# Kernel optimization log

Measured on AMD Instinct MI355X. Metric: run time of the kernel, lower is better.

## Reference

```python
import jax, jax.numpy as jnp
import numpy as np

NUM_HEADS = 16

def setup_inputs() -> dict:
    key = jax.random.key(0)
    k1, k2, k3, k4 = jax.random.split(key, 4)
    B, N, C = 4, 2048, 1024
    x = jax.random.normal(k1, (B, N, C), dtype=jnp.float32)
    xpos = jax.random.randint(k2, (B, N), 0, 2048, dtype=jnp.int64)
    Wqkv = jax.random.normal(k3, (C, 3 * C), dtype=jnp.float32) * (C ** -0.5)
    Wproj = jax.random.normal(k4, (C, C), dtype=jnp.float32) * (C ** -0.5)
    bproj = jnp.zeros((C,), dtype=jnp.float32)
    return {"x": x, "xpos": xpos, "Wqkv": Wqkv, "Wproj": Wproj, "bproj": bproj}

def reference(x, xpos, Wqkv, Wproj, bproj):
    # rope is None in this configuration, so xpos is unused (matches torch default path).
    B, N, C = x.shape
    H = NUM_HEADS
    Dh = C // H
    scale = Dh ** -0.5
    qkv = jnp.einsum('bnc,cd->bnd', x, Wqkv)              # [B, N, 3C]
    qkv = qkv.reshape(B, N, 3, H, Dh)
    q, k, v = qkv[:, :, 0], qkv[:, :, 1], qkv[:, :, 2]    # [B, N, H, Dh]
    scores = jnp.einsum('bnhd,bmhd->bhnm', q, k) * scale  # [B, H, N, N]
    attn = jax.nn.softmax(scores, axis=-1)
    out = jnp.einsum('bhnm,bmhd->bnhd', attn, v)          # [B, N, H, Dh]
    out = out.reshape(B, N, C)
    return jnp.einsum('bnc,cd->bnd', out, Wproj) + bproj
```

## Files before the change

kernel.cpp:

```cpp
#include <hip/hip_runtime.h>
#include <stdint.h>

#define DEVINL __device__ __forceinline__

typedef __bf16 bf16x8 __attribute__((ext_vector_type(8)));
typedef float f32x4 __attribute__((ext_vector_type(4)));
typedef float f32x16 __attribute__((ext_vector_type(16)));
typedef uint32_t u32x4 __attribute__((ext_vector_type(4)));

DEVINL uint16_t f2bf(float f) {
    uint32_t u = __builtin_bit_cast(uint32_t, f);
    uint32_t r = (u + 0x7FFFu + ((u >> 16) & 1u)) >> 16;
    return (uint16_t)r;
}

DEVINL bf16x8 ld8(const uint16_t* p) {
    u32x4 v = *(const u32x4*)p;
    return __builtin_bit_cast(bf16x8, v);
}

DEVINL void gload16(const void* g, void* l) {
    __builtin_amdgcn_global_load_lds(
        (const __attribute__((address_space(1))) uint32_t*)g,
        (__attribute__((address_space(3))) uint32_t*)l, 16, 0, 0);
}

DEVINL uint32_t cvtpk(float lo, float hi) {
    uint32_t r;
    asm("v_cvt_pk_bf16_f32 %0, %1, %2" : "=v"(r) : "v"(lo), "v"(hi));
    return r;
}

DEVINL float exp2_fast(float x) {
    float r;
    asm("v_exp_f32 %0, %1" : "=v"(r) : "v"(x));
    return r;
}

__global__ void k_cvt_x(const float* __restrict__ x, uint16_t* __restrict__ xb, int n8) {
    int i = blockIdx.x * blockDim.x + threadIdx.x;
    if (i >= n8) return;
    const float4* src = (const float4*)x + (size_t)i * 2;
    float4 a = src[0], b = src[1];
    union { uint16_t u[8]; u32x4 v; } o;
    o.u[0] = f2bf(a.x); o.u[1] = f2bf(a.y); o.u[2] = f2bf(a.z); o.u[3] = f2bf(a.w);
    o.u[4] = f2bf(b.x); o.u[5] = f2bf(b.y); o.u[6] = f2bf(b.z); o.u[7] = f2bf(b.w);
    ((u32x4*)xb)[i] = o.v;
}

__global__ void k_transW(const float* __restrict__ W, uint16_t* __restrict__ WT, int Nn) {
    __shared__ uint16_t t[64 * 65];
    int k0 = blockIdx.y * 64, n0 = blockIdx.x * 64;
    int tid = threadIdx.x;
#pragma unroll
    for (int i = 0; i < 4; ++i) {
        int c = tid + i * 256;
        int kr = c >> 4, nc = c & 15;
        float4 v = *(const float4*)(W + (size_t)(k0 + kr) * Nn + n0 + nc * 4);
        t[(nc * 4 + 0) * 65 + kr] = f2bf(v.x);
        t[(nc * 4 + 1) * 65 + kr] = f2bf(v.y);
        t[(nc * 4 + 2) * 65 + kr] = f2bf(v.z);
        t[(nc * 4 + 3) * 65 + kr] = f2bf(v.w);
    }
    __syncthreads();
#pragma unroll
    for (int i = 0; i < 2; ++i) {
        int c = tid + i * 256;
        int nr = c >> 3, kc = c & 7;
        union { uint16_t u[8]; u32x4 v; } o;
#pragma unroll
        for (int j = 0; j < 8; ++j) o.u[j] = t[nr * 65 + kc * 8 + j];
        *(u32x4*)(WT + (size_t)(n0 + nr) * 1024 + k0 + kc * 8) = o.v;
    }
}

__global__ void k_transV(const uint16_t* __restrict__ vn, uint16_t* __restrict__ vt) {
    __shared__ uint16_t t[64 * 65];
    int bh = blockIdx.y;
    int n0 = blockIdx.x * 64;
    int tid = threadIdx.x;
#pragma unroll
    for (int i = 0; i < 2; ++i) {
        int c = tid + i * 256;
        int n = c >> 3, dc = c & 7;
        u32x4 vv = *(const u32x4*)(vn + ((size_t)bh * 2048 + n0 + n) * 64 + dc * 8);
        union { u32x4 v4; uint16_t u[8]; } in; in.v4 = vv;
#pragma unroll
        for (int j = 0; j < 8; ++j) t[(dc * 8 + j) * 65 + n] = in.u[j];
    }
    __syncthreads();
#pragma unroll
    for (int i = 0; i < 2; ++i) {
        int c = tid + i * 256;
        int dh = c >> 3, nc = c & 7;
        union { uint16_t u[8]; u32x4 v4; } o;
#pragma unroll
        for (int j = 0; j < 8; ++j) o.u[j] = t[dh * 65 + nc * 8 + j];
        *(u32x4*)(vt + ((size_t)bh * 64 + dh) * 2048 + n0 + nc * 8) = o.v4;
    }
}

template <int MODE>
__global__ __launch_bounds__(256) void k_gemm(
    const uint16_t* __restrict__ A, const uint16_t* __restrict__ BT,
    const float* __restrict__ bias,
    uint16_t* __restrict__ qo, uint16_t* __restrict__ ko, uint16_t* __restrict__ vo,
    float* __restrict__ out) {
    __shared__ uint16_t a_lds[128 * 64];
    __shared__ uint16_t b_lds[128 * 64];
    int tid = threadIdx.x;
    int w = tid >> 6, l = tid & 63;
    int l15 = l & 15, l4 = l >> 4;
    int m0 = blockIdx.y * 128, n0 = blockIdx.x * 128;
    int wr = w >> 1, wc = w & 1;
    f32x4 acc[4][4] = {};

    for (int kt = 0; kt < 16; ++kt) {
#pragma unroll
        for (int i = 0; i < 4; ++i) {
            int c = i * 256 + w * 64 + l;
            int row = c >> 3, slot = c & 7;
            int kc = slot ^ (row & 7);
            gload16(A + (size_t)(m0 + row) * 1024 + kt * 64 + kc * 8,
                    a_lds + (size_t)(i * 256 + w * 64) * 8);
            gload16(BT + (size_t)(n0 + row) * 1024 + kt * 64 + kc * 8,
                    b_lds + (size_t)(i * 256 + w * 64) * 8);
        }
        __syncthreads();
#pragma unroll
        for (int kkk = 0; kkk < 2; ++kkk) {
            bf16x8 af[4], bfr[4];
#pragma unroll
            for (int i = 0; i < 4; ++i) {
                int row = wr * 64 + i * 16 + l15;
                af[i] = ld8(a_lds + row * 64 + ((kkk * 4 + l4) ^ (row & 7)) * 8);
                int rowb = wc * 64 + i * 16 + l15;
                bfr[i] = ld8(b_lds + rowb * 64 + ((kkk * 4 + l4) ^ (rowb & 7)) * 8);
            }
#pragma unroll
            for (int i = 0; i < 4; ++i)
#pragma unroll
                for (int j = 0; j < 4; ++j)
                    acc[i][j] = __builtin_amdgcn_mfma_f32_16x16x32_bf16(
                        af[i], bfr[j], acc[i][j], 0, 0, 0);
        }
        __syncthreads();
    }

    if constexpr (MODE == 0) {
#pragma unroll
        for (int i = 0; i < 4; ++i)
#pragma unroll
            for (int j = 0; j < 4; ++j) {
                int d = n0 + wc * 64 + j * 16 + l15;
                int s = d >> 10, h = (d >> 6) & 15, dh = d & 63;
                uint16_t* dst0 = (s == 0) ? qo : (s == 1) ? ko : vo;
                float sc = (s == 0) ? 0.18033688011112042f : 1.0f;
#pragma unroll
                for (int r = 0; r < 4; ++r) {
                    int m = m0 + wr * 64 + i * 16 + l4 * 4 + r;
                    int b = m >> 11, n = m & 2047;
                    dst0[((size_t)(b * 16 + h) * 2048 + n) * 64 + dh] = f2bf(acc[i][j][r] * sc);
                }
            }
    } else {
#pragma unroll
        for (int j = 0; j < 4; ++j) {
            int d = n0 + wc * 64 + j * 16 + l15;
            float bv = bias[d];
#pragma unroll
            for (int i = 0; i < 4; ++i)
#pragma unroll
                for (int r = 0; r < 4; ++r) {
                    int m = m0 + wr * 64 + i * 16 + l4 * 4 + r;
                    out[(size_t)m * 1024 + d] = acc[i][j][r] + bv;
                }
        }
    }
}

__global__ __launch_bounds__(256) void k_attn(
    const uint16_t* __restrict__ q, const uint16_t* __restrict__ kk_,
    const uint16_t* __restrict__ vt, uint16_t* __restrict__ o) {
    __shared__ uint16_t k_lds[2][64 * 64];
    __shared__ uint16_t v_lds[2][64 * 64];
    int tid = threadIdx.x;
    int w = tid >> 6, l = tid & 63;
    int l31 = l & 31, g = l >> 5;
    int bh = blockIdx.y;
    int qt = blockIdx.x;
    int qrow = qt * 128 + w * 32 + l31;
    const uint16_t* qb = q + ((size_t)bh * 2048 + qrow) * 64;
    const uint16_t* kbase = kk_ + (size_t)bh * 2048 * 64;
    const uint16_t* vbase = vt + (size_t)bh * 64 * 2048;

    bf16x8 qf[4];
#pragma unroll
    for (int kv = 0; kv < 4; ++kv) qf[kv] = ld8(qb + kv * 16 + g * 8);

    int c0 = w * 128 + l;
    int rr0 = c0 >> 3, sl0 = c0 & 7;
    int kc0 = sl0 ^ (rr0 & 7);
    int rr1 = rr0 + 8, kc1 = sl0 ^ (rr1 & 7);
    const uint16_t* kp0 = kbase + rr0 * 64 + kc0 * 8;
    const uint16_t* kp1 = kbase + rr1 * 64 + kc1 * 8;
    const uint16_t* vp0 = vbase + (size_t)rr0 * 2048 + kc0 * 8;
    const uint16_t* vp1 = vbase + (size_t)rr1 * 2048 + kc1 * 8;
    uint16_t* kd0 = k_lds[0] + w * 1024;
    uint16_t* kd1 = k_lds[1] + w * 1024;
    uint16_t* vd0 = v_lds[0] + w * 1024;
    uint16_t* vd1 = v_lds[1] + w * 1024;

    f32x16 oa[2] = {};
    f32x16 ls = {};
    u32x4 onesu; onesu[0] = onesu[1] = onesu[2] = onesu[3] = 0x3F803F80u;
    bf16x8 ones = __builtin_bit_cast(bf16x8, onesu);

    auto stage = [&](uint16_t* kd, uint16_t* vd) {
        gload16(kp0, kd);       gload16(kp1, kd + 512);
        gload16(vp0, vd);       gload16(vp1, vd + 512);
        kp0 += 4096; kp1 += 4096; vp0 += 64; vp1 += 64;
    };

    stage(kd0, vd0);
    asm volatile("s_waitcnt vmcnt(0)\n\ts_barrier" ::: "memory");

    auto body = [&](int t, const uint16_t* kb, const uint16_t* vb,
                    uint16_t* kdn, uint16_t* vdn) {
        if (t < 31) stage(kdn, vdn);

        bf16x8 pfrag[4];
#pragma unroll
        for (int j = 0; j < 2; ++j) {
            int key = j * 32 + l31;
            f32x16 stj = {};
            __builtin_amdgcn_s_setprio(1);
#pragma unroll
            for (int kv = 0; kv < 4; ++kv) {
                bf16x8 kf = ld8(kb + key * 64 + ((2 * kv + g) ^ (key & 7)) * 8);
                stj = __builtin_amdgcn_mfma_f32_32x32x16_bf16(kf, qf[kv], stj, 0, 0, 0);
            }
            __builtin_amdgcn_s_setprio(0);
#pragma unroll
            for (int h = 0; h < 2; ++h) {
                float e[8];
#pragma unroll
                for (int jj = 0; jj < 8; ++jj) e[jj] = exp2_fast(stj[h * 8 + jj]);
                uint32_t a0 = cvtpk(e[0], e[1]), a1 = cvtpk(e[2], e[3]);
                uint32_t b0 = cvtpk(e[4], e[5]), b1 = cvtpk(e[6], e[7]);
                auto r0 = __builtin_amdgcn_permlane32_swap(a0, b0, false, false);
                auto r1 = __builtin_amdgcn_permlane32_swap(a1, b1, false, false);
                u32x4 f;
                f[0] = r0[0]; f[1] = r1[0]; f[2] = r0[1]; f[3] = r1[1];
                pfrag[j * 2 + h] = __builtin_bit_cast(bf16x8, f);
            }
        }

        __builtin_amdgcn_s_setprio(1);
#pragma unroll
        for (int kv = 0; kv < 4; ++kv) {
            ls = __builtin_amdgcn_mfma_f32_32x32x16_bf16(ones, pfrag[kv], ls, 0, 0, 0);
#pragma unroll
            for (int dt = 0; dt < 2; ++dt) {
                int dh = dt * 32 + l31;
                bf16x8 vf = ld8(vb + dh * 64 + ((2 * kv + g) ^ (dh & 7)) * 8);
                oa[dt] = __builtin_amdgcn_mfma_f32_32x32x16_bf16(vf, pfrag[kv], oa[dt], 0, 0, 0);
            }
        }
        __builtin_amdgcn_s_setprio(0);
        asm volatile("s_waitcnt vmcnt(0)\n\ts_barrier" ::: "memory");
    };

    for (int kt = 0; kt < 32; kt += 2) {
        body(kt,     k_lds[0], v_lds[0], kd1, vd1);
        body(kt + 1, k_lds[1], v_lds[1], kd0, vd0);
    }

    float inv = 1.0f / ls[0];
    int b = bh >> 4, h = bh & 15;
    uint16_t* ob = o + ((size_t)(b * 2048 + qrow)) * 1024 + h * 64;
#pragma unroll
    for (int dt = 0; dt < 2; ++dt)
#pragma unroll
        for (int rq = 0; rq < 4; ++rq) {
            union { uint16_t u[4]; uint2 v; } pk;
#pragma unroll
            for (int rr = 0; rr < 4; ++rr) pk.u[rr] = f2bf(oa[dt][rq * 4 + rr] * inv);
            int dh0 = dt * 32 + rq * 8 + g * 4;
            *(uint2*)(ob + dh0) = pk.v;
        }
}

extern "C" void kernel_launch(void* const* d_in, const int* in_sizes, int n_in,
                              void* d_out, int out_size, void* d_ws, size_t ws_size,
                              hipStream_t stream) {
    const float* x     = (const float*)d_in[0];
    const float* Wqkv  = (const float*)d_in[2];
    const float* Wproj = (const float*)d_in[3];
    const float* bproj = (const float*)d_in[4];
    float* out = (float*)d_out;

    char* ws = (char*)d_ws;
    uint16_t* xb     = (uint16_t*)(ws);
    uint16_t* wqkvT  = (uint16_t*)(ws + 16777216);
    uint16_t* wprojT = (uint16_t*)(ws + 23068672);
    uint16_t* qws    = (uint16_t*)(ws + 25165824);
    uint16_t* kws    = (uint16_t*)(ws + 41943040);
    uint16_t* vT     = (uint16_t*)(ws + 58720256);
    uint16_t* vnat   = (uint16_t*)(ws + 75497472);
    uint16_t* attnout = xb;

    k_cvt_x<<<dim3(4096), dim3(256), 0, stream>>>(x, xb, 1048576);
    k_transW<<<dim3(48, 16), dim3(256), 0, stream>>>(Wqkv, wqkvT, 3072);
    k_transW<<<dim3(16, 16), dim3(256), 0, stream>>>(Wproj, wprojT, 1024);
    k_gemm<0><<<dim3(24, 64), dim3(256), 0, stream>>>(xb, wqkvT, nullptr, qws, kws, vnat, nullptr);
    k_transV<<<dim3(32, 64), dim3(256), 0, stream>>>(vnat, vT);
    k_attn<<<dim3(16, 64), dim3(256), 0, stream>>>(qws, kws, vT, attnout);
    k_gemm<1><<<dim3(8, 64), dim3(256), 0, stream>>>(attnout, wprojT, bproj, nullptr, nullptr, nullptr, out);
}
```

Before: 221.9 us.

## Process two 32-row query tiles per wave in attention kernel

Each wave now handles 64 query rows as two independent 32-row MFMA tiles that share each loaded K and V fragment from LDS. The attention grid is halved to 8 query blocks of 256 rows per head. This cuts LDS reads and global K/V staging per query row and gives the scheduler more independent MFMA work. In exchange it roughly doubles accumulator and fragment register pressure, which may lower occupancy, and launches half as many blocks (512).

```diff
diff --git a/kernel.cpp b/kernel.cpp
--- a/kernel.cpp
+++ b/kernel.cpp
@@ -189,14 +189,17 @@
     int l31 = l & 31, g = l >> 5;
     int bh = blockIdx.y;
     int qt = blockIdx.x;
-    int qrow = qt * 128 + w * 32 + l31;
+    int qrow = qt * 256 + w * 64 + l31;
     const uint16_t* qb = q + ((size_t)bh * 2048 + qrow) * 64;
     const uint16_t* kbase = kk_ + (size_t)bh * 2048 * 64;
     const uint16_t* vbase = vt + (size_t)bh * 64 * 2048;
 
-    bf16x8 qf[4];
-#pragma unroll
-    for (int kv = 0; kv < 4; ++kv) qf[kv] = ld8(qb + kv * 16 + g * 8);
+    bf16x8 qf0[4], qf1[4];
+#pragma unroll
+    for (int kv = 0; kv < 4; ++kv) {
+        qf0[kv] = ld8(qb + kv * 16 + g * 8);
+        qf1[kv] = ld8(qb + 2048 + kv * 16 + g * 8);
+    }
 
     int c0 = w * 128 + l;
     int rr0 = c0 >> 3, sl0 = c0 & 7;
@@ -211,8 +214,8 @@
     uint16_t* vd0 = v_lds[0] + w * 1024;
     uint16_t* vd1 = v_lds[1] + w * 1024;
 
-    f32x16 oa[2] = {};
-    f32x16 ls = {};
+    f32x16 oa0[2] = {}, oa1[2] = {};
+    f32x16 ls0 = {}, ls1 = {};
     u32x4 onesu; onesu[0] = onesu[1] = onesu[2] = onesu[3] = 0x3F803F80u;
     bf16x8 ones = __builtin_bit_cast(bf16x8, onesu);
 
@@ -229,42 +232,59 @@
                     uint16_t* kdn, uint16_t* vdn) {
         if (t < 31) stage(kdn, vdn);
 
-        bf16x8 pfrag[4];
+        bf16x8 pfrag0[4], pfrag1[4];
 #pragma unroll
         for (int j = 0; j < 2; ++j) {
             int key = j * 32 + l31;
-            f32x16 stj = {};
+            f32x16 st0 = {}, st1 = {};
             __builtin_amdgcn_s_setprio(1);
 #pragma unroll
             for (int kv = 0; kv < 4; ++kv) {
                 bf16x8 kf = ld8(kb + key * 64 + ((2 * kv + g) ^ (key & 7)) * 8);
-                stj = __builtin_amdgcn_mfma_f32_32x32x16_bf16(kf, qf[kv], stj, 0, 0, 0);
+                st0 = __builtin_amdgcn_mfma_f32_32x32x16_bf16(kf, qf0[kv], st0, 0, 0, 0);
+                st1 = __builtin_amdgcn_mfma_f32_32x32x16_bf16(kf, qf1[kv], st1, 0, 0, 0);
             }
             __builtin_amdgcn_s_setprio(0);
 #pragma unroll
             for (int h = 0; h < 2; ++h) {
-                float e[8];
-#pragma unroll
-                for (int jj = 0; jj < 8; ++jj) e[jj] = exp2_fast(stj[h * 8 + jj]);
-                uint32_t a0 = cvtpk(e[0], e[1]), a1 = cvtpk(e[2], e[3]);
-                uint32_t b0 = cvtpk(e[4], e[5]), b1 = cvtpk(e[6], e[7]);
-                auto r0 = __builtin_amdgcn_permlane32_swap(a0, b0, false, false);
-                auto r1 = __builtin_amdgcn_permlane32_swap(a1, b1, false, false);
-                u32x4 f;
-                f[0] = r0[0]; f[1] = r1[0]; f[2] = r0[1]; f[3] = r1[1];
-                pfrag[j * 2 + h] = __builtin_bit_cast(bf16x8, f);
+                {
+                    float e[8];
+#pragma unroll
+                    for (int jj = 0; jj < 8; ++jj) e[jj] = exp2_fast(st0[h * 8 + jj]);
+                    uint32_t a0 = cvtpk(e[0], e[1]), a1 = cvtpk(e[2], e[3]);
+                    uint32_t b0 = cvtpk(e[4], e[5]), b1 = cvtpk(e[6], e[7]);
+                    auto r0 = __builtin_amdgcn_permlane32_swap(a0, b0, false, false);
+                    auto r1 = __builtin_amdgcn_permlane32_swap(a1, b1, false, false);
+                    u32x4 f;
+                    f[0] = r0[0]; f[1] = r1[0]; f[2] = r0[1]; f[3] = r1[1];
+                    pfrag0[j * 2 + h] = __builtin_bit_cast(bf16x8, f);
+                }
+                {
+                    float e[8];
+#pragma unroll
+                    for (int jj = 0; jj < 8; ++jj) e[jj] = exp2_fast(st1[h * 8 + jj]);
+                    uint32_t a0 = cvtpk(e[0], e[1]), a1 = cvtpk(e[2], e[3]);
+                    uint32_t b0 = cvtpk(e[4], e[5]), b1 = cvtpk(e[6], e[7]);
+                    auto r0 = __builtin_amdgcn_permlane32_swap(a0, b0, false, false);
+                    auto r1 = __builtin_amdgcn_permlane32_swap(a1, b1, false, false);
+                    u32x4 f;
+                    f[0] = r0[0]; f[1] = r1[0]; f[2] = r0[1]; f[3] = r1[1];
+                    pfrag1[j * 2 + h] = __builtin_bit_cast(bf16x8, f);
+                }
             }
         }
 
         __builtin_amdgcn_s_setprio(1);
 #pragma unroll
         for (int kv = 0; kv < 4; ++kv) {
-            ls = __builtin_amdgcn_mfma_f32_32x32x16_bf16(ones, pfrag[kv], ls, 0, 0, 0);
+            ls0 = __builtin_amdgcn_mfma_f32_32x32x16_bf16(ones, pfrag0[kv], ls0, 0, 0, 0);
+            ls1 = __builtin_amdgcn_mfma_f32_32x32x16_bf16(ones, pfrag1[kv], ls1, 0, 0, 0);
 #pragma unroll
             for (int dt = 0; dt < 2; ++dt) {
                 int dh = dt * 32 + l31;
                 bf16x8 vf = ld8(vb + dh * 64 + ((2 * kv + g) ^ (dh & 7)) * 8);
-                oa[dt] = __builtin_amdgcn_mfma_f32_32x32x16_bf16(vf, pfrag[kv], oa[dt], 0, 0, 0);
+                oa0[dt] = __builtin_amdgcn_mfma_f32_32x32x16_bf16(vf, pfrag0[kv], oa0[dt], 0, 0, 0);
+                oa1[dt] = __builtin_amdgcn_mfma_f32_32x32x16_bf16(vf, pfrag1[kv], oa1[dt], 0, 0, 0);
             }
         }
         __builtin_amdgcn_s_setprio(0);
@@ -276,19 +296,35 @@
         body(kt + 1, k_lds[1], v_lds[1], kd0, vd0);
     }
 
-    float inv = 1.0f / ls[0];
-    int b = bh >> 4, h = bh & 15;
-    uint16_t* ob = o + ((size_t)(b * 2048 + qrow)) * 1024 + h * 64;
-#pragma unroll
-    for (int dt = 0; dt < 2; ++dt)
-#pragma unroll
-        for (int rq = 0; rq < 4; ++rq) {
-            union { uint16_t u[4]; uint2 v; } pk;
-#pragma unroll
-            for (int rr = 0; rr < 4; ++rr) pk.u[rr] = f2bf(oa[dt][rq * 4 + rr] * inv);
-            int dh0 = dt * 32 + rq * 8 + g * 4;
-            *(uint2*)(ob + dh0) = pk.v;
-        }
+    int b = bh >> 4, hh = bh & 15;
+    {
+        float inv = 1.0f / ls0[0];
+        uint16_t* ob = o + ((size_t)(b * 2048 + qrow)) * 1024 + hh * 64;
+#pragma unroll
+        for (int dt = 0; dt < 2; ++dt)
+#pragma unroll
+            for (int rq = 0; rq < 4; ++rq) {
+                union { uint16_t u[4]; uint2 v; } pk;
+#pragma unroll
+                for (int rr = 0; rr < 4; ++rr) pk.u[rr] = f2bf(oa0[dt][rq * 4 + rr] * inv);
+                int dh0 = dt * 32 + rq * 8 + g * 4;
+                *(uint2*)(ob + dh0) = pk.v;
+            }
+    }
+    {
+        float inv = 1.0f / ls1[0];
+        uint16_t* ob = o + ((size_t)(b * 2048 + qrow + 32)) * 1024 + hh * 64;
+#pragma unroll
+        for (int dt = 0; dt < 2; ++dt)
+#pragma unroll
+            for (int rq = 0; rq < 4; ++rq) {
+                union { uint16_t u[4]; uint2 v; } pk;
+#pragma unroll
+                for (int rr = 0; rr < 4; ++rr) pk.u[rr] = f2bf(oa1[dt][rq * 4 + rr] * inv);
+                int dh0 = dt * 32 + rq * 8 + g * 4;
+                *(uint2*)(ob + dh0) = pk.v;
+            }
+    }
 }
 
 extern "C" void kernel_launch(void* const* d_in, const int* in_sizes, int n_in,
@@ -315,6 +351,6 @@
     k_transW<<<dim3(16, 16), dim3(256), 0, stream>>>(Wproj, wprojT, 1024);
     k_gemm<0><<<dim3(24, 64), dim3(256), 0, stream>>>(xb, wqkvT, nullptr, qws, kws, vnat, nullptr);
     k_transV<<<dim3(32, 64), dim3(256), 0, stream>>>(vnat, vT);
-    k_attn<<<dim3(16, 64), dim3(256), 0, stream>>>(qws, kws, vT, attnout);
+    k_attn<<<dim3(8, 64), dim3(256), 0, stream>>>(qws, kws, vT, attnout);
     k_gemm<1><<<dim3(8, 64), dim3(256), 0, stream>>>(attnout, wprojT, bproj, nullptr, nullptr, nullptr, out);
 }
```

New measurement: 230.9 us. +4.0%, slower.

## Merge prep kernels into one launch and write V transposed from QKV GEMM

Applied to the files above, without the earlier changes.

Merges the x conversion and both weight transposes into a single k_prep launch that dispatches on block index. Removes the separate V transpose kernel by having the QKV GEMM epilogue write V directly in [bh, d, n] layout. This cuts two kernel launches and a full read and write of V. The price is uncoalesced strided stores for V in the GEMM epilogue, since consecutive lanes now write elements 2048 apart.

```diff
diff --git a/kernel.cpp b/kernel.cpp
--- a/kernel.cpp
+++ b/kernel.cpp
@@ -37,21 +37,8 @@
     return r;
 }
 
-__global__ void k_cvt_x(const float* __restrict__ x, uint16_t* __restrict__ xb, int n8) {
-    int i = blockIdx.x * blockDim.x + threadIdx.x;
-    if (i >= n8) return;
-    const float4* src = (const float4*)x + (size_t)i * 2;
-    float4 a = src[0], b = src[1];
-    union { uint16_t u[8]; u32x4 v; } o;
-    o.u[0] = f2bf(a.x); o.u[1] = f2bf(a.y); o.u[2] = f2bf(a.z); o.u[3] = f2bf(a.w);
-    o.u[4] = f2bf(b.x); o.u[5] = f2bf(b.y); o.u[6] = f2bf(b.z); o.u[7] = f2bf(b.w);
-    ((u32x4*)xb)[i] = o.v;
-}
-
-__global__ void k_transW(const float* __restrict__ W, uint16_t* __restrict__ WT, int Nn) {
-    __shared__ uint16_t t[64 * 65];
-    int k0 = blockIdx.y * 64, n0 = blockIdx.x * 64;
-    int tid = threadIdx.x;
+DEVINL void transW_body(const float* __restrict__ W, uint16_t* __restrict__ WT,
+                        int Nn, int n0, int k0, int tid, uint16_t* t) {
 #pragma unroll
     for (int i = 0; i < 4; ++i) {
         int c = tid + i * 256;
@@ -74,29 +61,26 @@
     }
 }
 
-__global__ void k_transV(const uint16_t* __restrict__ vn, uint16_t* __restrict__ vt) {
+__global__ void k_prep(const float* __restrict__ x, uint16_t* __restrict__ xb,
+                       const float* __restrict__ Wqkv, uint16_t* __restrict__ wqkvT,
+                       const float* __restrict__ Wproj, uint16_t* __restrict__ wprojT) {
     __shared__ uint16_t t[64 * 65];
-    int bh = blockIdx.y;
-    int n0 = blockIdx.x * 64;
+    int bid = blockIdx.x;
     int tid = threadIdx.x;
-#pragma unroll
-    for (int i = 0; i < 2; ++i) {
-        int c = tid + i * 256;
-        int n = c >> 3, dc = c & 7;
-        u32x4 vv = *(const u32x4*)(vn + ((size_t)bh * 2048 + n0 + n) * 64 + dc * 8);
-        union { u32x4 v4; uint16_t u[8]; } in; in.v4 = vv;
-#pragma unroll
-        for (int j = 0; j < 8; ++j) t[(dc * 8 + j) * 65 + n] = in.u[j];
-    }
-    __syncthreads();
-#pragma unroll
-    for (int i = 0; i < 2; ++i) {
-        int c = tid + i * 256;
-        int dh = c >> 3, nc = c & 7;
-        union { uint16_t u[8]; u32x4 v4; } o;
-#pragma unroll
-        for (int j = 0; j < 8; ++j) o.u[j] = t[dh * 65 + nc * 8 + j];
-        *(u32x4*)(vt + ((size_t)bh * 64 + dh) * 2048 + n0 + nc * 8) = o.v4;
+    if (bid < 4096) {
+        int i = bid * 256 + tid;
+        const float4* src = (const float4*)x + (size_t)i * 2;
+        float4 a = src[0], b = src[1];
+        union { uint16_t u[8]; u32x4 v; } o;
+        o.u[0] = f2bf(a.x); o.u[1] = f2bf(a.y); o.u[2] = f2bf(a.z); o.u[3] = f2bf(a.w);
+        o.u[4] = f2bf(b.x); o.u[5] = f2bf(b.y); o.u[6] = f2bf(b.z); o.u[7] = f2bf(b.w);
+        ((u32x4*)xb)[i] = o.v;
+    } else if (bid < 4864) {
+        int idx = bid - 4096;
+        transW_body(Wqkv, wqkvT, 3072, (idx % 48) * 64, (idx / 48) * 64, tid, t);
+    } else {
+        int idx = bid - 4864;
+        transW_body(Wproj, wprojT, 1024, (idx % 16) * 64, (idx / 16) * 64, tid, t);
     }
 }
 
@@ -154,13 +138,18 @@
             for (int j = 0; j < 4; ++j) {
                 int d = n0 + wc * 64 + j * 16 + l15;
                 int s = d >> 10, h = (d >> 6) & 15, dh = d & 63;
-                uint16_t* dst0 = (s == 0) ? qo : (s == 1) ? ko : vo;
                 float sc = (s == 0) ? 0.18033688011112042f : 1.0f;
 #pragma unroll
                 for (int r = 0; r < 4; ++r) {
                     int m = m0 + wr * 64 + i * 16 + l4 * 4 + r;
                     int b = m >> 11, n = m & 2047;
-                    dst0[((size_t)(b * 16 + h) * 2048 + n) * 64 + dh] = f2bf(acc[i][j][r] * sc);
+                    uint16_t val = f2bf(acc[i][j][r] * sc);
+                    if (s == 2) {
+                        vo[((size_t)(b * 16 + h) * 64 + dh) * 2048 + n] = val;
+                    } else {
+                        uint16_t* dst0 = (s == 0) ? qo : ko;
+                        dst0[((size_t)(b * 16 + h) * 2048 + n) * 64 + dh] = val;
+                    }
                 }
             }
     } else {
@@ -307,14 +296,10 @@
     uint16_t* qws    = (uint16_t*)(ws + 25165824);
     uint16_t* kws    = (uint16_t*)(ws + 41943040);
     uint16_t* vT     = (uint16_t*)(ws + 58720256);
-    uint16_t* vnat   = (uint16_t*)(ws + 75497472);
     uint16_t* attnout = xb;
 
-    k_cvt_x<<<dim3(4096), dim3(256), 0, stream>>>(x, xb, 1048576);
-    k_transW<<<dim3(48, 16), dim3(256), 0, stream>>>(Wqkv, wqkvT, 3072);
-    k_transW<<<dim3(16, 16), dim3(256), 0, stream>>>(Wproj, wprojT, 1024);
-    k_gemm<0><<<dim3(24, 64), dim3(256), 0, stream>>>(xb, wqkvT, nullptr, qws, kws, vnat, nullptr);
-    k_transV<<<dim3(32, 64), dim3(256), 0, stream>>>(vnat, vT);
+    k_prep<<<dim3(5120), dim3(256), 0, stream>>>(x, xb, Wqkv, wqkvT, Wproj, wprojT);
+    k_gemm<0><<<dim3(24, 64), dim3(256), 0, stream>>>(xb, wqkvT, nullptr, qws, kws, vT, nullptr);
     k_attn<<<dim3(16, 64), dim3(256), 0, stream>>>(qws, kws, vT, attnout);
     k_gemm<1><<<dim3(8, 64), dim3(256), 0, stream>>>(attnout, wprojT, bproj, nullptr, nullptr, nullptr, out);
 }
```

Measured after the change: 236.8 us. +6.7%, slower.
